# Kernel tuning notes

Measured on AMD Instinct MI355X. Metric: run time of the kernel, lower is better.

Reference implementation:

```python
import jax, jax.numpy as jnp
import numpy as np

B, P, N, M = 8, 50, 128, 128          # batch, pomo, query nodes, route tokens
EMB, H, D = 128, 8, 16                # embedding_dim, head_num, qkv_dim
NE, K = 8, 2                          # num_experts, top-k
CLIP = 10.0                           # logit_clipping


def setup_inputs() -> dict:
    key = jax.random.key(0)
    ks = jax.random.split(key, 12)
    s = 0.02
    return {
        "encoded_nodes": jax.random.normal(ks[0], (B, P, N, EMB), jnp.float32),
        "encoded_routes": jax.random.normal(ks[1], (B, P, M, EMB + 1), jnp.float32),
        "ninf_mask": jnp.zeros((B, P, N), jnp.float32),
        "route_mask": jnp.zeros((B, P, N, M), jnp.float32),
        "Wq": s * jax.random.normal(ks[2], (EMB, H * D), jnp.float32),
        "Wk": s * jax.random.normal(ks[3], (EMB + 1, H * D), jnp.float32),
        "Wv": s * jax.random.normal(ks[4], (EMB + 1, H * D), jnp.float32),
        "Wg": s * jax.random.normal(ks[5], (H * D, NE), jnp.float32),
        "We": s * jax.random.normal(ks[6], (NE, H * D, EMB + 1), jnp.float32),
        "be": jnp.zeros((NE, EMB + 1), jnp.float32),
        "Wfinal": s * jax.random.normal(ks[7], (EMB + 1, 1), jnp.float32),
    }


def _heads(x, W):
    # x: [B,P,n,F] @ W[F,H*D] -> [B,P,H,n,D]
    y = x @ W
    b, p, n, _ = y.shape
    return jnp.swapaxes(y.reshape(b, p, n, H, D), 2, 3)


def reference(encoded_nodes, encoded_routes, ninf_mask, route_mask,
              Wq, Wk, Wv, Wg, We, be, Wfinal):
    # --- masked multi-head attention (multi_head_attention1) ---
    q = _heads(encoded_nodes, Wq)          # [B,P,H,N,D]
    k = _heads(encoded_routes, Wk)         # [B,P,H,M,D]
    v = _heads(encoded_routes, Wv)         # [B,P,H,M,D]
    score = jnp.einsum('bphnd,bphmd->bphnm', q, k) / jnp.sqrt(jnp.float32(D))
    score = score + route_mask[:, :, None, :, :]          # rank3 ninf mask
    w = jax.nn.softmax(score, axis=-1)
    # rank2 mask applied multiplicatively after softmax
    keep = jnp.where(ninf_mask == 0.0, 1.0, 0.0)[:, :, None, :, None]
    w = w * keep
    out = jnp.einsum('bphnm,bphmd->bphnd', w, v)
    out_concat = jnp.swapaxes(out, 2, 3).reshape(B, P, N, H * D)

    # --- top-k gated MoE combine (noisy gating, eval: no noise) ---
    x = out_concat.reshape(-1, H * D)                     # [T, H*D]
    T = x.shape[0]
    gate_logits = x @ Wg                                  # [T, NE]
    top_vals, top_idx = jax.lax.top_k(gate_logits, K)
    top_g = jax.nn.softmax(top_vals, axis=-1)
    gates = jnp.zeros((T, NE), x.dtype).at[jnp.arange(T)[:, None], top_idx].set(top_g)
    expert_out = jnp.einsum('ti,eio->teo', x, We) + be    # [T, NE, EMB+1]
    moe_out = jnp.einsum('te,teo->to', gates, expert_out)
    importance = gates.sum(0)
    moe_loss = importance.var() / (importance.mean() ** 2 + 1e-10)
    mh_atten_out = moe_out.reshape(B, P, N, EMB + 1)

    # --- final scoring ---
    score_scaled = (mh_atten_out @ Wfinal)[..., 0]        # [B,P,N]
    score_clipped = CLIP * jnp.tanh(score_scaled)
    score_masked = score_clipped + ninf_mask
    probs = jax.nn.softmax(score_masked, axis=2)
    return probs, moe_loss
```

## Files before the change

### kernel.cpp

```cpp
#include <hip/hip_runtime.h>

constexpr int B  = 8,  P = 50, N = 128, M = 128;
constexpr int EMB = 128, H = 8, D = 16;
constexpr int NE = 8;
constexpr int HD = H * D;
constexpr int E1 = EMB + 1;
constexpr int BP = B * P;
constexpr int T  = BP * N;

__global__ void prep_kernel(const float* __restrict__ We,
                            const float* __restrict__ be,
                            const float* __restrict__ Wf,
                            float* __restrict__ Wep, float* __restrict__ bpv,
                            float* __restrict__ importance) {
    const int e = blockIdx.x;
    const int f = threadIdx.x;

    float a = 0.f;
    const long base = ((long)e * HD + f) * E1;
    for (int o = 0; o < E1; ++o) a += We[base + o] * Wf[o];
    Wep[e * HD + f] = a;

    if (f == 0) {
        float b = 0.f;
        for (int o = 0; o < E1; ++o) b += be[(long)e * E1 + o] * Wf[o];
        bpv[e] = b;
    }
    if (e == 0 && f < NE) importance[f] = 0.f;
}

__global__ __launch_bounds__(256) void proj_kernel(
    const float* __restrict__ nodes,
    const float* __restrict__ routes,
    const float* __restrict__ Wq, const float* __restrict__ Wk,
    const float* __restrict__ Wv,
    float* __restrict__ qo, float* __restrict__ ko, float* __restrict__ vo) {
    const int mat = blockIdx.y;
    const float* __restrict__ X = (mat == 0) ? nodes : routes;
    const float* __restrict__ W = (mat == 0) ? Wq : (mat == 1 ? Wk : Wv);
    float* __restrict__ out     = (mat == 0) ? qo : (mat == 1 ? ko : vo);
    const int Kd = (mat == 0) ? EMB : E1;
    const int nit = (Kd + 7) >> 3;

    const int row0 = blockIdx.x * 128;
    const int tid  = threadIdx.x;
    const int tr   = tid >> 4;
    const int tc   = tid & 15;

    __shared__ float XT[2][8][132];
    __shared__ float WS[2][8][132];

    float acc[8][8];
    #pragma unroll
    for (int i = 0; i < 8; ++i)
        #pragma unroll
        for (int j = 0; j < 8; ++j) acc[i][j] = 0.f;

    float xr[4];
    float4 wr;
    const int xkx = tid & 7, xrr = tid >> 3;
    const int wkx = tid >> 5, wc4 = (tid & 31) * 4;

    {
        #pragma unroll
        for (int i = 0; i < 4; ++i) {
            int kg = xkx;
            xr[i] = (kg < Kd) ? X[(long)(row0 + xrr + i * 32) * Kd + kg] : 0.f;
        }
        wr = (wkx < Kd) ? *(const float4*)&W[(long)wkx * HD + wc4]
                        : make_float4(0.f, 0.f, 0.f, 0.f);
        #pragma unroll
        for (int i = 0; i < 4; ++i) XT[0][xkx][xrr + i * 32] = xr[i];
        *(float4*)&WS[0][wkx][wc4] = wr;
    }
    __syncthreads();

    for (int it = 0; it < nit; ++it) {
        const int buf = it & 1;
        if (it + 1 < nit) {
            const int kk = (it + 1) * 8;
            #pragma unroll
            for (int i = 0; i < 4; ++i) {
                int kg = kk + xkx;
                xr[i] = (kg < Kd) ? X[(long)(row0 + xrr + i * 32) * Kd + kg] : 0.f;
            }
            int kg = kk + wkx;
            wr = (kg < Kd) ? *(const float4*)&W[(long)kg * HD + wc4]
                           : make_float4(0.f, 0.f, 0.f, 0.f);
        }

        #pragma unroll
        for (int k = 0; k < 8; ++k) {
            float4 xa = *(const float4*)&XT[buf][k][tr * 4];
            float4 xb = *(const float4*)&XT[buf][k][64 + tr * 4];
            float4 wa = *(const float4*)&WS[buf][k][tc * 4];
            float4 wb = *(const float4*)&WS[buf][k][64 + tc * 4];
            float xv[8] = {xa.x, xa.y, xa.z, xa.w, xb.x, xb.y, xb.z, xb.w};
            float wv[8] = {wa.x, wa.y, wa.z, wa.w, wb.x, wb.y, wb.z, wb.w};
            #pragma unroll
            for (int i = 0; i < 8; ++i)
                #pragma unroll
                for (int j = 0; j < 8; ++j) acc[i][j] += xv[i] * wv[j];
        }

        if (it + 1 < nit) {
            const int nb = buf ^ 1;
            #pragma unroll
            for (int i = 0; i < 4; ++i) XT[nb][xkx][xrr + i * 32] = xr[i];
            *(float4*)&WS[nb][wkx][wc4] = wr;
        }
        __syncthreads();
    }

    #pragma unroll
    for (int i = 0; i < 8; ++i) {
        int r = row0 + (i < 4 ? 0 : 64) + tr * 4 + (i & 3);
        float4 o0 = make_float4(acc[i][0], acc[i][1], acc[i][2], acc[i][3]);
        float4 o1 = make_float4(acc[i][4], acc[i][5], acc[i][6], acc[i][7]);
        *(float4*)&out[(long)r * HD + tc * 4]      = o0;
        *(float4*)&out[(long)r * HD + 64 + tc * 4] = o1;
    }
}

__global__ __launch_bounds__(64) void attn_kernel(
    const float* __restrict__ qbuf,
    const float* __restrict__ kbuf,
    const float* __restrict__ vbuf,
    const float* __restrict__ rmask,
    const float* __restrict__ ninf,
    float* __restrict__ xcat) {
    const int bp  = blockIdx.x;
    const int h   = blockIdx.y;
    const int tid = threadIdx.x;

    __shared__ float kh[M][D];
    __shared__ float vh[M][D];

    #pragma unroll
    for (int i = 0; i < 8; ++i) {
        int e = tid + i * 64;
        int r = e >> 2, c4 = (e & 3) * 4;
        *(float4*)&kh[r][c4] = *(const float4*)&kbuf[((long)bp * M + r) * HD + h * D + c4];
        *(float4*)&vh[r][c4] = *(const float4*)&vbuf[((long)bp * M + r) * HD + h * D + c4];
    }
    __syncthreads();

    const long t0 = (long)bp * N + tid, t1 = t0 + 64;

    float qr0[16], qr1[16];
    {
        const float4* q0 = (const float4*)&qbuf[t0 * HD + h * D];
        const float4* q1 = (const float4*)&qbuf[t1 * HD + h * D];
        #pragma unroll
        for (int i = 0; i < 4; ++i) {
            float4 a = q0[i], b = q1[i];
            qr0[i*4+0] = a.x*0.25f; qr0[i*4+1] = a.y*0.25f;
            qr0[i*4+2] = a.z*0.25f; qr0[i*4+3] = a.w*0.25f;
            qr1[i*4+0] = b.x*0.25f; qr1[i*4+1] = b.y*0.25f;
            qr1[i*4+2] = b.z*0.25f; qr1[i*4+3] = b.w*0.25f;
        }
    }

    const float4* rm0 = (const float4*)&rmask[t0 * M];
    const float4* rm1 = (const float4*)&rmask[t1 * M];

    float sum0 = 0.f, sum1 = 0.f;
    float o0[16], o1[16];
    #pragma unroll
    for (int d = 0; d < 16; ++d) { o0[d] = 0.f; o1[d] = 0.f; }

    for (int mb = 0; mb < 32; ++mb) {
        float4 r0 = rm0[mb], r1 = rm1[mb];
        float r0v[4] = {r0.x, r0.y, r0.z, r0.w};
        float r1v[4] = {r1.x, r1.y, r1.z, r1.w};
        #pragma unroll
        for (int j = 0; j < 4; ++j) {
            const int m = mb * 4 + j;
            const float4* k4 = (const float4*)&kh[m][0];
            const float4* v4 = (const float4*)&vh[m][0];
            float s0 = 0.f, s1 = 0.f;
            #pragma unroll
            for (int q4 = 0; q4 < 4; ++q4) {
                float4 kq = k4[q4];
                s0 += qr0[q4*4+0]*kq.x + qr0[q4*4+1]*kq.y
                    + qr0[q4*4+2]*kq.z + qr0[q4*4+3]*kq.w;
                s1 += qr1[q4*4+0]*kq.x + qr1[q4*4+1]*kq.y
                    + qr1[q4*4+2]*kq.z + qr1[q4*4+3]*kq.w;
            }
            float e0 = __expf(s0 + r0v[j]);
            float e1 = __expf(s1 + r1v[j]);
            sum0 += e0; sum1 += e1;
            #pragma unroll
            for (int q4 = 0; q4 < 4; ++q4) {
                float4 vq = v4[q4];
                o0[q4*4+0] += e0*vq.x; o0[q4*4+1] += e0*vq.y;
                o0[q4*4+2] += e0*vq.z; o0[q4*4+3] += e0*vq.w;
                o1[q4*4+0] += e1*vq.x; o1[q4*4+1] += e1*vq.y;
                o1[q4*4+2] += e1*vq.z; o1[q4*4+3] += e1*vq.w;
            }
        }
    }

    const float inv0 = ((ninf[t0] == 0.f) ? 1.f : 0.f) / sum0;
    const float inv1 = ((ninf[t1] == 0.f) ? 1.f : 0.f) / sum1;
    #pragma unroll
    for (int q4 = 0; q4 < 4; ++q4) {
        float4 w0 = make_float4(o0[q4*4+0]*inv0, o0[q4*4+1]*inv0,
                                o0[q4*4+2]*inv0, o0[q4*4+3]*inv0);
        float4 w1 = make_float4(o1[q4*4+0]*inv1, o1[q4*4+1]*inv1,
                                o1[q4*4+2]*inv1, o1[q4*4+3]*inv1);
        *(float4*)&xcat[t0 * HD + h * D + q4 * 4] = w0;
        *(float4*)&xcat[t1 * HD + h * D + q4 * 4] = w1;
    }
}

__global__ __launch_bounds__(128) void moe_final_kernel(
    const float* __restrict__ xcat, const float* __restrict__ Wg,
    const float* __restrict__ ninf, const float* __restrict__ Wep,
    const float* __restrict__ bpv, float* __restrict__ importance,
    float* __restrict__ out) {
    __shared__ float WgS[EMB][NE];
    __shared__ float WeS[NE][132];
    __shared__ float red[N];
    __shared__ float impS[NE];

    const int bp = blockIdx.x;
    const int n  = threadIdx.x;

    #pragma unroll
    for (int i = 0; i < 2; ++i) {
        int e = n + i * 128;
        int r = e >> 1, c4 = (e & 1) * 4;
        *(float4*)&WgS[r][c4] = *(const float4*)&Wg[(long)r * NE + c4];
    }
    #pragma unroll
    for (int i = 0; i < 2; ++i) {
        int idx = n + i * 128;
        int r = idx >> 5, c = (idx & 31) * 4;
        *(float4*)&WeS[r][c] = *(const float4*)&Wep[(long)r * HD + c];
    }
    if (n < NE) impS[n] = 0.f;
    __syncthreads();

    const long t = (long)bp * N + n;
    const float4* row4 = (const float4*)&xcat[t * HD];

    float gl[NE];
    #pragma unroll
    for (int e = 0; e < NE; ++e) gl[e] = 0.f;
    for (int fb = 0; fb < 32; ++fb) {
        float4 xv = row4[fb];
        float x4[4] = {xv.x, xv.y, xv.z, xv.w};
        #pragma unroll
        for (int j = 0; j < 4; ++j)
            #pragma unroll
            for (int e = 0; e < NE; ++e) gl[e] += x4[j] * WgS[fb * 4 + j][e];
    }

    int e0 = 0; float v0 = gl[0];
    #pragma unroll
    for (int e = 1; e < NE; ++e) if (gl[e] > v0) { v0 = gl[e]; e0 = e; }
    int e1 = -1; float v1 = -3.4e38f;
    #pragma unroll
    for (int e = 0; e < NE; ++e) if (e != e0 && gl[e] > v1) { v1 = gl[e]; e1 = e; }
    float ex = __expf(v1 - v0);
    float g0 = 1.f / (1.f + ex);
    float g1 = ex / (1.f + ex);

    atomicAdd(&impS[e0], g0);
    atomicAdd(&impS[e1], g1);

    float s = g0 * bpv[e0] + g1 * bpv[e1];
    for (int fb = 0; fb < 32; ++fb) {
        float4 xv = row4[fb];
        float x4[4] = {xv.x, xv.y, xv.z, xv.w};
        #pragma unroll
        for (int j = 0; j < 4; ++j) {
            int f = fb * 4 + j;
            s += x4[j] * (g0 * WeS[e0][f] + g1 * WeS[e1][f]);
        }
    }
    s = 10.f * tanhf(s) + ninf[t];

    red[n] = s;
    __syncthreads();
    for (int off = 64; off > 0; off >>= 1) {
        if (n < off) red[n] = fmaxf(red[n], red[n + off]);
        __syncthreads();
    }
    float mx = red[0];
    __syncthreads();
    float e = __expf(s - mx);
    red[n] = e;
    __syncthreads();
    for (int off = 64; off > 0; off >>= 1) {
        if (n < off) red[n] += red[n + off];
        __syncthreads();
    }
    float sum = red[0];

    out[t] = e / sum;

    if (n < NE) atomicAdd(&importance[n], impS[n]);
}

__global__ void loss_kernel(const float* __restrict__ importance,
                            float* __restrict__ out) {
    if (threadIdx.x == 0) {
        float mean = 0.f;
        #pragma unroll
        for (int e = 0; e < NE; ++e) mean += importance[e];
        mean *= (1.f / NE);
        float var = 0.f;
        #pragma unroll
        for (int e = 0; e < NE; ++e) {
            float d = importance[e] - mean;
            var += d * d;
        }
        var *= (1.f / NE);
        out[T] = var / (mean * mean + 1e-10f);
    }
}

extern "C" void kernel_launch(void* const* d_in, const int* in_sizes, int n_in,
                              void* d_out, int out_size, void* d_ws, size_t ws_size,
                              hipStream_t stream) {
    const float* nodes  = (const float*)d_in[0];
    const float* routes = (const float*)d_in[1];
    const float* ninf   = (const float*)d_in[2];
    const float* rmask  = (const float*)d_in[3];
    const float* Wq     = (const float*)d_in[4];
    const float* Wk     = (const float*)d_in[5];
    const float* Wv     = (const float*)d_in[6];
    const float* Wg     = (const float*)d_in[7];
    const float* We     = (const float*)d_in[8];
    const float* be     = (const float*)d_in[9];
    const float* Wfin   = (const float*)d_in[10];

    float* ws = (float*)d_ws;
    float* Wep        = ws + 16;
    float* bpv        = ws + 1040;
    float* importance = ws + 1048;
    float* qbuf       = ws + 4096;
    float* kbuf       = qbuf + (long)T * HD;
    float* vbuf       = kbuf + (long)T * HD;
    float* xcat       = vbuf + (long)T * HD;

    float* out = (float*)d_out;

    prep_kernel<<<NE, 128, 0, stream>>>(We, be, Wfin, Wep, bpv, importance);
    proj_kernel<<<dim3(400, 3), 256, 0, stream>>>(nodes, routes, Wq, Wk, Wv,
                                                  qbuf, kbuf, vbuf);
    attn_kernel<<<dim3(BP, H), 64, 0, stream>>>(qbuf, kbuf, vbuf,
                                                rmask, ninf, xcat);
    moe_final_kernel<<<BP, 128, 0, stream>>>(xcat, Wg, ninf, Wep, bpv,
                                             importance, out);
    loss_kernel<<<1, 64, 0, stream>>>(importance, out);
}
```

Baseline: 305.3 us.

## Use direct global-to-LDS loads for weights and double-buffered K/V chunks

The projection kernel now loads its weight tile straight into LDS with global_load_lds instead of staging it through registers, and the weight tile loses its padding. The attention kernel streams K/V in double-buffered 32-row chunks via direct-to-LDS loads, so copying overlaps with compute instead of loading everything up front. The grid order is swapped so all heads of one batch-pomo run next to each other, which should improve cache locality for q and the mask. No explicit wait on the async LDS loads appears before __syncthreads, so correctness depends on the compiler inserting the vmcnt waits.

Result: slower. 340.7 us (+11.6%).

```diff
diff --git a/kernel.cpp b/kernel.cpp
--- a/kernel.cpp
+++ b/kernel.cpp
@@ -7,6 +7,13 @@
 constexpr int E1 = EMB + 1;
 constexpr int BP = B * P;
 constexpr int T  = BP * N;
+
+__device__ __forceinline__ void dma16(const float* g, float* l) {
+    __builtin_amdgcn_global_load_lds(
+        (const __attribute__((address_space(1))) void*)g,
+        (__attribute__((address_space(3))) void*)l,
+        16, 0, 0);
+}
 
 __global__ void prep_kernel(const float* __restrict__ We,
                             const float* __restrict__ be,
@@ -48,7 +55,7 @@
     const int tc   = tid & 15;
 
     __shared__ float XT[2][8][132];
-    __shared__ float WS[2][8][132];
+    __shared__ float WS[2][8][128];
 
     float acc[8][8];
     #pragma unroll
@@ -57,21 +64,21 @@
         for (int j = 0; j < 8; ++j) acc[i][j] = 0.f;
 
     float xr[4];
-    float4 wr;
     const int xkx = tid & 7, xrr = tid >> 3;
-    const int wkx = tid >> 5, wc4 = (tid & 31) * 4;
+    const int wv   = tid >> 6;
+    const int lane = tid & 63;
+    const int wkrow = 2 * wv + (lane >> 5);
+    const int wcol  = (lane & 31) * 4;
 
     {
+        if (wkrow < Kd) dma16(&W[(long)wkrow * HD + wcol], &WS[0][2 * wv][0]);
         #pragma unroll
         for (int i = 0; i < 4; ++i) {
             int kg = xkx;
             xr[i] = (kg < Kd) ? X[(long)(row0 + xrr + i * 32) * Kd + kg] : 0.f;
         }
-        wr = (wkx < Kd) ? *(const float4*)&W[(long)wkx * HD + wc4]
-                        : make_float4(0.f, 0.f, 0.f, 0.f);
         #pragma unroll
         for (int i = 0; i < 4; ++i) XT[0][xkx][xrr + i * 32] = xr[i];
-        *(float4*)&WS[0][wkx][wc4] = wr;
     }
     __syncthreads();
 
@@ -79,14 +86,13 @@
         const int buf = it & 1;
         if (it + 1 < nit) {
             const int kk = (it + 1) * 8;
+            int kgw = kk + wkrow;
+            if (kgw < Kd) dma16(&W[(long)kgw * HD + wcol], &WS[buf ^ 1][2 * wv][0]);
             #pragma unroll
             for (int i = 0; i < 4; ++i) {
                 int kg = kk + xkx;
                 xr[i] = (kg < Kd) ? X[(long)(row0 + xrr + i * 32) * Kd + kg] : 0.f;
             }
-            int kg = kk + wkx;
-            wr = (kg < Kd) ? *(const float4*)&W[(long)kg * HD + wc4]
-                           : make_float4(0.f, 0.f, 0.f, 0.f);
         }
 
         #pragma unroll
@@ -96,18 +102,17 @@
             float4 wa = *(const float4*)&WS[buf][k][tc * 4];
             float4 wb = *(const float4*)&WS[buf][k][64 + tc * 4];
             float xv[8] = {xa.x, xa.y, xa.z, xa.w, xb.x, xb.y, xb.z, xb.w};
-            float wv[8] = {wa.x, wa.y, wa.z, wa.w, wb.x, wb.y, wb.z, wb.w};
+            float wvv[8] = {wa.x, wa.y, wa.z, wa.w, wb.x, wb.y, wb.z, wb.w};
             #pragma unroll
             for (int i = 0; i < 8; ++i)
                 #pragma unroll
-                for (int j = 0; j < 8; ++j) acc[i][j] += xv[i] * wv[j];
+                for (int j = 0; j < 8; ++j) acc[i][j] += xv[i] * wvv[j];
         }
 
         if (it + 1 < nit) {
             const int nb = buf ^ 1;
             #pragma unroll
             for (int i = 0; i < 4; ++i) XT[nb][xkx][xrr + i * 32] = xr[i];
-            *(float4*)&WS[nb][wkx][wc4] = wr;
         }
         __syncthreads();
     }
@@ -129,21 +134,23 @@
     const float* __restrict__ rmask,
     const float* __restrict__ ninf,
     float* __restrict__ xcat) {
-    const int bp  = blockIdx.x;
-    const int h   = blockIdx.y;
+    const int h   = blockIdx.x;
+    const int bp  = blockIdx.y;
     const int tid = threadIdx.x;
 
-    __shared__ float kh[M][D];
-    __shared__ float vh[M][D];
-
-    #pragma unroll
-    for (int i = 0; i < 8; ++i) {
-        int e = tid + i * 64;
-        int r = e >> 2, c4 = (e & 3) * 4;
-        *(float4*)&kh[r][c4] = *(const float4*)&kbuf[((long)bp * M + r) * HD + h * D + c4];
-        *(float4*)&vh[r][c4] = *(const float4*)&vbuf[((long)bp * M + r) * HD + h * D + c4];
-    }
-    __syncthreads();
+    __shared__ float kc[2][32][16];
+    __shared__ float vc[2][32][16];
+
+    const float* __restrict__ kbase = kbuf + ((long)bp * M) * HD + h * D;
+    const float* __restrict__ vbase = vbuf + ((long)bp * M) * HD + h * D;
+
+    const int sr = tid >> 2;
+    const int sc = (tid & 3) * 4;
+
+    dma16(&kbase[(long)(sr)      * HD + sc], &kc[0][0][0]);
+    dma16(&kbase[(long)(sr + 16) * HD + sc], &kc[0][16][0]);
+    dma16(&vbase[(long)(sr)      * HD + sc], &vc[0][0][0]);
+    dma16(&vbase[(long)(sr + 16) * HD + sc], &vc[0][16][0]);
 
     const long t0 = (long)bp * N + tid, t1 = t0 + 64;
 
@@ -169,36 +176,52 @@
     #pragma unroll
     for (int d = 0; d < 16; ++d) { o0[d] = 0.f; o1[d] = 0.f; }
 
-    for (int mb = 0; mb < 32; ++mb) {
-        float4 r0 = rm0[mb], r1 = rm1[mb];
-        float r0v[4] = {r0.x, r0.y, r0.z, r0.w};
-        float r1v[4] = {r1.x, r1.y, r1.z, r1.w};
-        #pragma unroll
-        for (int j = 0; j < 4; ++j) {
-            const int m = mb * 4 + j;
-            const float4* k4 = (const float4*)&kh[m][0];
-            const float4* v4 = (const float4*)&vh[m][0];
-            float s0 = 0.f, s1 = 0.f;
-            #pragma unroll
-            for (int q4 = 0; q4 < 4; ++q4) {
-                float4 kq = k4[q4];
-                s0 += qr0[q4*4+0]*kq.x + qr0[q4*4+1]*kq.y
-                    + qr0[q4*4+2]*kq.z + qr0[q4*4+3]*kq.w;
-                s1 += qr1[q4*4+0]*kq.x + qr1[q4*4+1]*kq.y
-                    + qr1[q4*4+2]*kq.z + qr1[q4*4+3]*kq.w;
+    __syncthreads();
+
+    for (int c = 0; c < 4; ++c) {
+        const int b = c & 1;
+        if (c < 3) {
+            const int r0 = (c + 1) * 32 + sr;
+            dma16(&kbase[(long)(r0)      * HD + sc], &kc[b ^ 1][0][0]);
+            dma16(&kbase[(long)(r0 + 16) * HD + sc], &kc[b ^ 1][16][0]);
+            dma16(&vbase[(long)(r0)      * HD + sc], &vc[b ^ 1][0][0]);
+            dma16(&vbase[(long)(r0 + 16) * HD + sc], &vc[b ^ 1][16][0]);
+        }
+
+        #pragma unroll
+        for (int mbl = 0; mbl < 8; ++mbl) {
+            const int mb = c * 8 + mbl;
+            float4 r0 = rm0[mb], r1 = rm1[mb];
+            float r0v[4] = {r0.x, r0.y, r0.z, r0.w};
+            float r1v[4] = {r1.x, r1.y, r1.z, r1.w};
+            #pragma unroll
+            for (int j = 0; j < 4; ++j) {
+                const int ml = mbl * 4 + j;
+                const float4* k4 = (const float4*)&kc[b][ml][0];
+                const float4* v4 = (const float4*)&vc[b][ml][0];
+                float s0 = 0.f, s1 = 0.f;
+                #pragma unroll
+                for (int q4 = 0; q4 < 4; ++q4) {
+                    float4 kq = k4[q4];
+                    s0 += qr0[q4*4+0]*kq.x + qr0[q4*4+1]*kq.y
+                        + qr0[q4*4+2]*kq.z + qr0[q4*4+3]*kq.w;
+                    s1 += qr1[q4*4+0]*kq.x + qr1[q4*4+1]*kq.y
+                        + qr1[q4*4+2]*kq.z + qr1[q4*4+3]*kq.w;
+                }
+                float e0 = __expf(s0 + r0v[j]);
+                float e1 = __expf(s1 + r1v[j]);
+                sum0 += e0; sum1 += e1;
+                #pragma unroll
+                for (int q4 = 0; q4 < 4; ++q4) {
+                    float4 vq = v4[q4];
+                    o0[q4*4+0] += e0*vq.x; o0[q4*4+1] += e0*vq.y;
+                    o0[q4*4+2] += e0*vq.z; o0[q4*4+3] += e0*vq.w;
+                    o1[q4*4+0] += e1*vq.x; o1[q4*4+1] += e1*vq.y;
+                    o1[q4*4+2] += e1*vq.z; o1[q4*4+3] += e1*vq.w;
+                }
             }
-            float e0 = __expf(s0 + r0v[j]);
-            float e1 = __expf(s1 + r1v[j]);
-            sum0 += e0; sum1 += e1;
-            #pragma unroll
-            for (int q4 = 0; q4 < 4; ++q4) {
-                float4 vq = v4[q4];
-                o0[q4*4+0] += e0*vq.x; o0[q4*4+1] += e0*vq.y;
-                o0[q4*4+2] += e0*vq.z; o0[q4*4+3] += e0*vq.w;
-                o1[q4*4+0] += e1*vq.x; o1[q4*4+1] += e1*vq.y;
-                o1[q4*4+2] += e1*vq.z; o1[q4*4+3] += e1*vq.w;
-            }
-        }
+        }
+        __syncthreads();
     }
 
     const float inv0 = ((ninf[t0] == 0.f) ? 1.f : 0.f) / sum0;
@@ -351,7 +374,7 @@
     prep_kernel<<<NE, 128, 0, stream>>>(We, be, Wfin, Wep, bpv, importance);
     proj_kernel<<<dim3(400, 3), 256, 0, stream>>>(nodes, routes, Wq, Wk, Wv,
                                                   qbuf, kbuf, vbuf);
-    attn_kernel<<<dim3(BP, H), 64, 0, stream>>>(qbuf, kbuf, vbuf,
+    attn_kernel<<<dim3(H, BP), 64, 0, stream>>>(qbuf, kbuf, vbuf,
                                                 rmask, ninf, xcat);
     moe_final_kernel<<<BP, 128, 0, stream>>>(xcat, Wg, ninf, Wep, bpv,
                                              importance, out);
```

## Chunk attention K/V staging and split MoE gating from row softmax

Applied to the files above, without the earlier changes.

The attention kernel now stages K/V in two 64-row chunks instead of the full 128 rows, halving its shared memory so more blocks can be resident per CU. The MoE/final kernel is split in two. A gate kernel runs 256 tokens per block over 200 blocks and writes the clipped scores to a workspace buffer. A separate softmax kernel then does the per-row normalization. This adds an extra launch, a global round-trip for the scores, and extra barriers in the attention loop.

New measurement: 385.8 us. +26.4%, slower.

```diff
diff --git a/kernel.cpp b/kernel.cpp
--- a/kernel.cpp
+++ b/kernel.cpp
@@ -96,11 +96,11 @@
             float4 wa = *(const float4*)&WS[buf][k][tc * 4];
             float4 wb = *(const float4*)&WS[buf][k][64 + tc * 4];
             float xv[8] = {xa.x, xa.y, xa.z, xa.w, xb.x, xb.y, xb.z, xb.w};
-            float wv[8] = {wa.x, wa.y, wa.z, wa.w, wb.x, wb.y, wb.z, wb.w};
+            float wvv[8] = {wa.x, wa.y, wa.z, wa.w, wb.x, wb.y, wb.z, wb.w};
             #pragma unroll
             for (int i = 0; i < 8; ++i)
                 #pragma unroll
-                for (int j = 0; j < 8; ++j) acc[i][j] += xv[i] * wv[j];
+                for (int j = 0; j < 8; ++j) acc[i][j] += xv[i] * wvv[j];
         }
 
         if (it + 1 < nit) {
@@ -133,17 +133,8 @@
     const int h   = blockIdx.y;
     const int tid = threadIdx.x;
 
-    __shared__ float kh[M][D];
-    __shared__ float vh[M][D];
-
-    #pragma unroll
-    for (int i = 0; i < 8; ++i) {
-        int e = tid + i * 64;
-        int r = e >> 2, c4 = (e & 3) * 4;
-        *(float4*)&kh[r][c4] = *(const float4*)&kbuf[((long)bp * M + r) * HD + h * D + c4];
-        *(float4*)&vh[r][c4] = *(const float4*)&vbuf[((long)bp * M + r) * HD + h * D + c4];
-    }
-    __syncthreads();
+    __shared__ float kh[64][16];
+    __shared__ float vh[64][16];
 
     const long t0 = (long)bp * N + tid, t1 = t0 + 64;
 
@@ -169,36 +160,51 @@
     #pragma unroll
     for (int d = 0; d < 16; ++d) { o0[d] = 0.f; o1[d] = 0.f; }
 
-    for (int mb = 0; mb < 32; ++mb) {
-        float4 r0 = rm0[mb], r1 = rm1[mb];
-        float r0v[4] = {r0.x, r0.y, r0.z, r0.w};
-        float r1v[4] = {r1.x, r1.y, r1.z, r1.w};
-        #pragma unroll
-        for (int j = 0; j < 4; ++j) {
-            const int m = mb * 4 + j;
-            const float4* k4 = (const float4*)&kh[m][0];
-            const float4* v4 = (const float4*)&vh[m][0];
-            float s0 = 0.f, s1 = 0.f;
-            #pragma unroll
-            for (int q4 = 0; q4 < 4; ++q4) {
-                float4 kq = k4[q4];
-                s0 += qr0[q4*4+0]*kq.x + qr0[q4*4+1]*kq.y
-                    + qr0[q4*4+2]*kq.z + qr0[q4*4+3]*kq.w;
-                s1 += qr1[q4*4+0]*kq.x + qr1[q4*4+1]*kq.y
-                    + qr1[q4*4+2]*kq.z + qr1[q4*4+3]*kq.w;
+    for (int c = 0; c < 2; ++c) {
+        #pragma unroll
+        for (int i = 0; i < 4; ++i) {
+            int e = tid + i * 64;
+            int r = e >> 2, c4 = (e & 3) * 4;
+            long grow = (long)bp * M + c * 64 + r;
+            *(float4*)&kh[r][c4] = *(const float4*)&kbuf[grow * HD + h * D + c4];
+            *(float4*)&vh[r][c4] = *(const float4*)&vbuf[grow * HD + h * D + c4];
+        }
+        __syncthreads();
+
+        #pragma unroll
+        for (int mbl = 0; mbl < 16; ++mbl) {
+            const int mb = c * 16 + mbl;
+            float4 r0 = rm0[mb], r1 = rm1[mb];
+            float r0v[4] = {r0.x, r0.y, r0.z, r0.w};
+            float r1v[4] = {r1.x, r1.y, r1.z, r1.w};
+            #pragma unroll
+            for (int j = 0; j < 4; ++j) {
+                const int ml = mbl * 4 + j;
+                const float4* k4 = (const float4*)&kh[ml][0];
+                const float4* v4 = (const float4*)&vh[ml][0];
+                float s0 = 0.f, s1 = 0.f;
+                #pragma unroll
+                for (int q4 = 0; q4 < 4; ++q4) {
+                    float4 kq = k4[q4];
+                    s0 += qr0[q4*4+0]*kq.x + qr0[q4*4+1]*kq.y
+                        + qr0[q4*4+2]*kq.z + qr0[q4*4+3]*kq.w;
+                    s1 += qr1[q4*4+0]*kq.x + qr1[q4*4+1]*kq.y
+                        + qr1[q4*4+2]*kq.z + qr1[q4*4+3]*kq.w;
+                }
+                float e0 = __expf(s0 + r0v[j]);
+                float e1 = __expf(s1 + r1v[j]);
+                sum0 += e0; sum1 += e1;
+                #pragma unroll
+                for (int q4 = 0; q4 < 4; ++q4) {
+                    float4 vq = v4[q4];
+                    o0[q4*4+0] += e0*vq.x; o0[q4*4+1] += e0*vq.y;
+                    o0[q4*4+2] += e0*vq.z; o0[q4*4+3] += e0*vq.w;
+                    o1[q4*4+0] += e1*vq.x; o1[q4*4+1] += e1*vq.y;
+                    o1[q4*4+2] += e1*vq.z; o1[q4*4+3] += e1*vq.w;
+                }
             }
-            float e0 = __expf(s0 + r0v[j]);
-            float e1 = __expf(s1 + r1v[j]);
-            sum0 += e0; sum1 += e1;
-            #pragma unroll
-            for (int q4 = 0; q4 < 4; ++q4) {
-                float4 vq = v4[q4];
-                o0[q4*4+0] += e0*vq.x; o0[q4*4+1] += e0*vq.y;
-                o0[q4*4+2] += e0*vq.z; o0[q4*4+3] += e0*vq.w;
-                o1[q4*4+0] += e1*vq.x; o1[q4*4+1] += e1*vq.y;
-                o1[q4*4+2] += e1*vq.z; o1[q4*4+3] += e1*vq.w;
-            }
-        }
+        }
+        __syncthreads();
     }
 
     const float inv0 = ((ninf[t0] == 0.f) ? 1.f : 0.f) / sum0;
@@ -214,35 +220,28 @@
     }
 }
 
-__global__ __launch_bounds__(128) void moe_final_kernel(
+__global__ __launch_bounds__(256) void gate_kernel(
     const float* __restrict__ xcat, const float* __restrict__ Wg,
-    const float* __restrict__ ninf, const float* __restrict__ Wep,
-    const float* __restrict__ bpv, float* __restrict__ importance,
-    float* __restrict__ out) {
+    const float* __restrict__ Wep, const float* __restrict__ bpv,
+    float* __restrict__ importance, float* __restrict__ sbuf) {
     __shared__ float WgS[EMB][NE];
     __shared__ float WeS[NE][132];
-    __shared__ float red[N];
     __shared__ float impS[NE];
 
-    const int bp = blockIdx.x;
-    const int n  = threadIdx.x;
-
-    #pragma unroll
-    for (int i = 0; i < 2; ++i) {
-        int e = n + i * 128;
-        int r = e >> 1, c4 = (e & 1) * 4;
+    const int tid = threadIdx.x;
+
+    {
+        int r = tid >> 1, c4 = (tid & 1) * 4;
         *(float4*)&WgS[r][c4] = *(const float4*)&Wg[(long)r * NE + c4];
     }
-    #pragma unroll
-    for (int i = 0; i < 2; ++i) {
-        int idx = n + i * 128;
-        int r = idx >> 5, c = (idx & 31) * 4;
+    {
+        int r = tid >> 5, c = (tid & 31) * 4;
         *(float4*)&WeS[r][c] = *(const float4*)&Wep[(long)r * HD + c];
     }
-    if (n < NE) impS[n] = 0.f;
-    __syncthreads();
-
-    const long t = (long)bp * N + n;
+    if (tid < NE) impS[tid] = 0.f;
+    __syncthreads();
+
+    const long t = (long)blockIdx.x * 256 + tid;
     const float4* row4 = (const float4*)&xcat[t * HD];
 
     float gl[NE];
@@ -280,8 +279,21 @@
             s += x4[j] * (g0 * WeS[e0][f] + g1 * WeS[e1][f]);
         }
     }
-    s = 10.f * tanhf(s) + ninf[t];
-
+    sbuf[t] = 10.f * tanhf(s);
+
+    __syncthreads();
+    if (tid < NE) atomicAdd(&importance[tid], impS[tid]);
+}
+
+__global__ __launch_bounds__(128) void softmax_kernel(
+    const float* __restrict__ sbuf, const float* __restrict__ ninf,
+    float* __restrict__ out) {
+    __shared__ float red[N];
+    const int bp = blockIdx.x;
+    const int n  = threadIdx.x;
+    const long t = (long)bp * N + n;
+
+    float s = sbuf[t] + ninf[t];
     red[n] = s;
     __syncthreads();
     for (int off = 64; off > 0; off >>= 1) {
@@ -297,11 +309,7 @@
         if (n < off) red[n] += red[n + off];
         __syncthreads();
     }
-    float sum = red[0];
-
-    out[t] = e / sum;
-
-    if (n < NE) atomicAdd(&importance[n], impS[n]);
+    out[t] = e / red[0];
 }
 
 __global__ void loss_kernel(const float* __restrict__ importance,
@@ -345,6 +353,7 @@
     float* kbuf       = qbuf + (long)T * HD;
     float* vbuf       = kbuf + (long)T * HD;
     float* xcat       = vbuf + (long)T * HD;
+    float* sbuf       = xcat + (long)T * HD;
 
     float* out = (float*)d_out;
 
@@ -353,7 +362,7 @@
                                                   qbuf, kbuf, vbuf);
     attn_kernel<<<dim3(BP, H), 64, 0, stream>>>(qbuf, kbuf, vbuf,
                                                 rmask, ninf, xcat);
-    moe_final_kernel<<<BP, 128, 0, stream>>>(xcat, Wg, ninf, Wep, bpv,
-                                             importance, out);
+    gate_kernel<<<200, 256, 0, stream>>>(xcat, Wg, Wep, bpv, importance, sbuf);
+    softmax_kernel<<<BP, 128, 0, stream>>>(sbuf, ninf, out);
     loss_kernel<<<1, 64, 0, stream>>>(importance, out);
 }
```

## Split attention key loop across two wavefronts with LDS reduction

Applied to the files above, without the earlier changes.

The attention kernel now launches 128 threads per block. Each of the two wavefronts loads and processes half of the 128 route tokens for the same 128 queries, then combines the partial softmax sums and outputs through shared memory. This halves the serial per-thread loop over keys and doubles the wavefronts available for latency hiding. The cost is an extra LDS reduction, two barriers, and an idle second wavefront during the final normalisation and store.

Measured after the change: 307.1 us. About the same (+0.6%).

```diff
diff --git a/kernel.cpp b/kernel.cpp
--- a/kernel.cpp
+++ b/kernel.cpp
@@ -96,11 +96,11 @@
             float4 wa = *(const float4*)&WS[buf][k][tc * 4];
             float4 wb = *(const float4*)&WS[buf][k][64 + tc * 4];
             float xv[8] = {xa.x, xa.y, xa.z, xa.w, xb.x, xb.y, xb.z, xb.w};
-            float wv[8] = {wa.x, wa.y, wa.z, wa.w, wb.x, wb.y, wb.z, wb.w};
+            float wvv[8] = {wa.x, wa.y, wa.z, wa.w, wb.x, wb.y, wb.z, wb.w};
             #pragma unroll
             for (int i = 0; i < 8; ++i)
                 #pragma unroll
-                for (int j = 0; j < 8; ++j) acc[i][j] += xv[i] * wv[j];
+                for (int j = 0; j < 8; ++j) acc[i][j] += xv[i] * wvv[j];
         }
 
         if (it + 1 < nit) {
@@ -122,30 +122,32 @@
     }
 }
 
-__global__ __launch_bounds__(64) void attn_kernel(
+__global__ __launch_bounds__(128) void attn_kernel(
     const float* __restrict__ qbuf,
     const float* __restrict__ kbuf,
     const float* __restrict__ vbuf,
     const float* __restrict__ rmask,
     const float* __restrict__ ninf,
     float* __restrict__ xcat) {
-    const int bp  = blockIdx.x;
-    const int h   = blockIdx.y;
-    const int tid = threadIdx.x;
-
-    __shared__ float kh[M][D];
-    __shared__ float vh[M][D];
-
-    #pragma unroll
-    for (int i = 0; i < 8; ++i) {
-        int e = tid + i * 64;
+    const int bp   = blockIdx.x;
+    const int h    = blockIdx.y;
+    const int tid  = threadIdx.x;
+    const int w    = tid >> 6;
+    const int lane = tid & 63;
+
+    __shared__ float kh[2][64][16];
+    __shared__ float vh[2][64][16];
+
+    #pragma unroll
+    for (int i = 0; i < 4; ++i) {
+        int e = lane + i * 64;
         int r = e >> 2, c4 = (e & 3) * 4;
-        *(float4*)&kh[r][c4] = *(const float4*)&kbuf[((long)bp * M + r) * HD + h * D + c4];
-        *(float4*)&vh[r][c4] = *(const float4*)&vbuf[((long)bp * M + r) * HD + h * D + c4];
-    }
-    __syncthreads();
-
-    const long t0 = (long)bp * N + tid, t1 = t0 + 64;
+        long grow = (long)bp * M + w * 64 + r;
+        *(float4*)&kh[w][r][c4] = *(const float4*)&kbuf[grow * HD + h * D + c4];
+        *(float4*)&vh[w][r][c4] = *(const float4*)&vbuf[grow * HD + h * D + c4];
+    }
+
+    const long t0 = (long)bp * N + lane, t1 = t0 + 64;
 
     float qr0[16], qr1[16];
     {
@@ -169,15 +171,16 @@
     #pragma unroll
     for (int d = 0; d < 16; ++d) { o0[d] = 0.f; o1[d] = 0.f; }
 
-    for (int mb = 0; mb < 32; ++mb) {
+    for (int mbl = 0; mbl < 16; ++mbl) {
+        const int mb = w * 16 + mbl;
         float4 r0 = rm0[mb], r1 = rm1[mb];
         float r0v[4] = {r0.x, r0.y, r0.z, r0.w};
         float r1v[4] = {r1.x, r1.y, r1.z, r1.w};
         #pragma unroll
         for (int j = 0; j < 4; ++j) {
-            const int m = mb * 4 + j;
-            const float4* k4 = (const float4*)&kh[m][0];
-            const float4* v4 = (const float4*)&vh[m][0];
+            const int ml = mbl * 4 + j;
+            const float4* k4 = (const float4*)&kh[w][ml][0];
+            const float4* v4 = (const float4*)&vh[w][ml][0];
             float s0 = 0.f, s1 = 0.f;
             #pragma unroll
             for (int q4 = 0; q4 < 4; ++q4) {
@@ -201,16 +204,39 @@
         }
     }
 
-    const float inv0 = ((ninf[t0] == 0.f) ? 1.f : 0.f) / sum0;
-    const float inv1 = ((ninf[t1] == 0.f) ? 1.f : 0.f) / sum1;
-    #pragma unroll
-    for (int q4 = 0; q4 < 4; ++q4) {
-        float4 w0 = make_float4(o0[q4*4+0]*inv0, o0[q4*4+1]*inv0,
-                                o0[q4*4+2]*inv0, o0[q4*4+3]*inv0);
-        float4 w1 = make_float4(o1[q4*4+0]*inv1, o1[q4*4+1]*inv1,
-                                o1[q4*4+2]*inv1, o1[q4*4+3]*inv1);
-        *(float4*)&xcat[t0 * HD + h * D + q4 * 4] = w0;
-        *(float4*)&xcat[t1 * HD + h * D + q4 * 4] = w1;
+    __syncthreads();
+    float* c0 = &kh[0][0][0];
+    float* c1 = &vh[0][0][0];
+    if (w == 1) {
+        #pragma unroll
+        for (int d = 0; d < 16; ++d) {
+            c0[d * 64 + lane] = o0[d];
+            c1[d * 64 + lane] = o1[d];
+        }
+        c0[16 * 64 + lane] = sum0;
+        c1[16 * 64 + lane] = sum1;
+    }
+    __syncthreads();
+    if (w == 0) {
+        #pragma unroll
+        for (int d = 0; d < 16; ++d) {
+            o0[d] += c0[d * 64 + lane];
+            o1[d] += c1[d * 64 + lane];
+        }
+        sum0 += c0[16 * 64 + lane];
+        sum1 += c1[16 * 64 + lane];
+
+        const float inv0 = ((ninf[t0] == 0.f) ? 1.f : 0.f) / sum0;
+        const float inv1 = ((ninf[t1] == 0.f) ? 1.f : 0.f) / sum1;
+        #pragma unroll
+        for (int q4 = 0; q4 < 4; ++q4) {
+            float4 w0 = make_float4(o0[q4*4+0]*inv0, o0[q4*4+1]*inv0,
+                                    o0[q4*4+2]*inv0, o0[q4*4+3]*inv0);
+            float4 w1 = make_float4(o1[q4*4+0]*inv1, o1[q4*4+1]*inv1,
+                                    o1[q4*4+2]*inv1, o1[q4*4+3]*inv1);
+            *(float4*)&xcat[t0 * HD + h * D + q4 * 4] = w0;
+            *(float4*)&xcat[t1 * HD + h * D + q4 * 4] = w1;
+        }
     }
 }
 
@@ -351,8 +377,8 @@
     prep_kernel<<<NE, 128, 0, stream>>>(We, be, Wfin, Wep, bpv, importance);
     proj_kernel<<<dim3(400, 3), 256, 0, stream>>>(nodes, routes, Wq, Wk, Wv,
                                                   qbuf, kbuf, vbuf);
-    attn_kernel<<<dim3(BP, H), 64, 0, stream>>>(qbuf, kbuf, vbuf,
-                                                rmask, ninf, xcat);
+    attn_kernel<<<dim3(BP, H), 128, 0, stream>>>(qbuf, kbuf, vbuf,
+                                                 rmask, ninf, xcat);
     moe_final_kernel<<<BP, 128, 0, stream>>>(xcat, Wg, ninf, Wep, bpv,
                                              importance, out);
     loss_kernel<<<1, 64, 0, stream>>>(importance, out);
```
